# Kernel tuning notes

Measured on AMD Instinct MI355X. Metric: run time of the kernel, lower is better.

Reference implementation:

```python
import jax, jax.numpy as jnp
import numpy as np

MARGIN = 0.2
EPS = 1e-6  # F.pairwise_distance default eps (added to the difference)


def _cdist(x):
    # Euclidean pairwise distances, [N, N]
    sq = jnp.sum(x * x, axis=1)
    d2 = sq[:, None] + sq[None, :] - 2.0 * (x @ x.T)
    return jnp.sqrt(jnp.maximum(d2, 0.0))


def setup_inputs() -> dict:
    key = jax.random.key(0)
    k1, k2 = jax.random.split(key)
    features = jax.random.normal(k1, (8192, 128), dtype=jnp.float32)
    labels = jax.random.randint(k2, (8192,), 0, 512)
    return {"features": features, "labels": labels}


def reference(features, labels):
    # Distances are used only for (non-differentiable) index selection.
    dists = jax.lax.stop_gradient(_cdist(features))
    pos_mask = labels[None, :] == labels[:, None]  # includes diagonal (self), as in the torch loop
    neg_mask = ~pos_mask

    # Batch-hard mining, vectorized over all anchor rows:
    # hardest positive = max dist among same-label; hardest negative = min dist among different-label.
    pos_idx = jnp.argmax(jnp.where(pos_mask, dists, -jnp.inf), axis=1)
    neg_idx = jnp.argmin(jnp.where(neg_mask, dists, jnp.inf), axis=1)
    # Anchor is skipped in the original loop only if it has no negatives.
    valid = jnp.any(neg_mask, axis=1)

    anchors = features
    pos = features[pos_idx]
    neg = features[neg_idx]

    # F.pairwise_distance(x1, x2, p=2) == ||x1 - x2 + eps||_2
    pos_d = jnp.linalg.norm(anchors - pos + EPS, axis=1)
    neg_d = jnp.linalg.norm(anchors - neg + EPS, axis=1)
    per_anchor = jax.nn.relu(pos_d - neg_d + MARGIN)

    cnt = jnp.sum(valid)
    loss = jnp.where(
        cnt > 0,
        jnp.sum(jnp.where(valid, per_anchor, 0.0)) / jnp.maximum(cnt, 1).astype(per_anchor.dtype),
        jnp.zeros((), per_anchor.dtype),
    )
    return loss
```

## Files before the change

### kernel.cpp

```cpp
#include <hip/hip_runtime.h>
#include <hip/hip_bf16.h>

#define N 8192
#define DIMS 128
#define NSLICE 32
#define SLICE_COLS (N / NSLICE)
#define SUBTILES (SLICE_COLS / 16)
#define NSTEPS (SUBTILES / 2)
#define ROWS_PER_BLOCK 128
#define STRIPS 2
#define NROWBLK (N / ROWS_PER_BLOCK)
#define NFIN 2048
#define MARGIN_F 0.2f
#define EPS_F 1e-6f
#define META_LDS 16384
#define INF_F __builtin_huge_valf()

typedef __bf16 bf16x8 __attribute__((ext_vector_type(8)));
typedef float f32x4 __attribute__((ext_vector_type(4)));

#define XB_OFF   0
#define XNEG_OFF 2097152
#define META_OFF 4194304
#define PART_OFF 4259840
#define BSUM_OFF 6356992

#define GLD_LDS(g, l) \
  __builtin_amdgcn_global_load_lds( \
      (const __attribute__((address_space(1))) void*)(g), \
      (__attribute__((address_space(3))) void*)(l), 16, 0, 0)

__global__ __launch_bounds__(256) void prep_kernel(
    const float* __restrict__ feat, const int* __restrict__ lab,
    unsigned short* __restrict__ Xb, unsigned short* __restrict__ Xneg,
    float2* __restrict__ meta) {
  int row = blockIdx.x * 4 + (threadIdx.x >> 6);
  int lane = threadIdx.x & 63;
  float2 x = *reinterpret_cast<const float2*>(feat + (size_t)row * DIMS + lane * 2);
  __hip_bfloat16 hx = __float2bfloat16(x.x);
  __hip_bfloat16 hy = __float2bfloat16(x.y);
  unsigned short ux, uy;
  __builtin_memcpy(&ux, &hx, 2);
  __builtin_memcpy(&uy, &hy, 2);
  unsigned int packed = (unsigned int)ux | ((unsigned int)uy << 16);
  *reinterpret_cast<unsigned int*>(Xb + (size_t)row * DIMS + lane * 2) = packed;
  *reinterpret_cast<unsigned int*>(Xneg + (size_t)row * DIMS + lane * 2) =
      packed ^ 0x80008000u;
  float s = x.x * x.x + x.y * x.y;
#pragma unroll
  for (int m = 32; m >= 1; m >>= 1) s += __shfl_xor(s, m, 64);
  if (lane == 0)
    meta[row] = make_float2(0.5f * (s + 512.0f), __int_as_float(lab[row]));
}

__global__ __launch_bounds__(256, 4) void mine_kernel(
    const unsigned short* __restrict__ Xb, const unsigned short* __restrict__ Xneg,
    const float2* __restrict__ meta, const int* __restrict__ lab,
    uint2* __restrict__ part) {
  __shared__ char smem[2 * 8192 + 2048];

  int rb = blockIdx.x / NSLICE;
  int sl = blockIdx.x % NSLICE;
  int tid = threadIdx.x;
  int wave = tid >> 6;
  int lane = tid & 63;
  int lrow = lane & 15;
  int lk = lane >> 4;
  int rowbase = rb * ROWS_PER_BLOCK + wave * (STRIPS * 16);
  int j0 = sl * SLICE_COLS;

  if (wave < 2) {
    const char* g = (const char*)meta + (size_t)j0 * 8 + tid * 16;
    char* l = smem + META_LDS + wave * 1024;
    GLD_LDS(g, l);
  }
  int colt = tid >> 4;
  int chunk = tid & 15;
  const char* gsrc0 = (const char*)Xneg + (size_t)(j0 + colt) * 256 +
                      ((chunk ^ (colt & 7)) * 16);
  {
    GLD_LDS(gsrc0, smem + wave * 1024);
    GLD_LDS(gsrc0 + 4096, smem + 4096 + wave * 1024);
  }

  bf16x8 afrag[STRIPS][4];
#pragma unroll
  for (int s = 0; s < STRIPS; ++s) {
    const unsigned short* rp = Xb + (size_t)(rowbase + s * 16 + lrow) * DIMS;
#pragma unroll
    for (int g = 0; g < 4; ++g)
      afrag[s][g] = *reinterpret_cast<const bf16x8*>(rp + g * 32 + lk * 8);
  }
  int4 labi[STRIPS];
#pragma unroll
  for (int s = 0; s < STRIPS; ++s)
    labi[s] = *reinterpret_cast<const int4*>(lab + rowbase + s * 16 + lk * 4);

  unsigned int bpu[STRIPS][4], bnu[STRIPS][4];
#pragma unroll
  for (int s = 0; s < STRIPS; ++s)
#pragma unroll
    for (int e = 0; e < 4; ++e) { bpu[s][e] = 0u; bnu[s][e] = 0xFFFFFFFFu; }

  int boff[4];
#pragma unroll
  for (int g = 0; g < 4; ++g)
    boff[g] = lrow * 256 + (((g * 4 + lk) ^ (lrow & 7)) * 16);

  __syncthreads();

  for (int it = 0; it < NSTEPS; ++it) {
    int cur = it & 1;
    if (it + 1 < NSTEPS) {
      const char* g = gsrc0 + (size_t)(it + 1) * 8192;
      char* l = smem + (cur ^ 1) * 8192 + wave * 1024;
      GLD_LDS(g, l);
      GLD_LDS(g + 4096, l + 4096);
    }

#pragma unroll
    for (int h = 0; h < 2; ++h) {
      int t = it * 2 + h;
      float2 mcur =
          *reinterpret_cast<const float2*>(smem + META_LDS + t * 128 + lrow * 8);
      float hinit = mcur.x;
      int labj = __float_as_int(mcur.y);
      unsigned int ju = (unsigned int)(j0 + t * 16 + lrow);

      const char* bbase = smem + cur * 8192 + h * 4096;
      bf16x8 bb[4];
#pragma unroll
      for (int g = 0; g < 4; ++g)
        bb[g] = *reinterpret_cast<const bf16x8*>(bbase + boff[g]);

#pragma unroll
      for (int s = 0; s < STRIPS; ++s) {
        f32x4 acc = {hinit, hinit, hinit, hinit};
#pragma unroll
        for (int g = 0; g < 4; ++g)
          acc = __builtin_amdgcn_mfma_f32_16x16x32_bf16(afrag[s][g], bb[g], acc,
                                                        0, 0, 0);
        int labs[4] = {labi[s].x, labi[s].y, labi[s].z, labi[s].w};
#pragma unroll
        for (int e = 0; e < 4; ++e) {
          unsigned int u = (__float_as_uint(acc[e]) & 0xFFFFE000u) | ju;
          bool pos = (labj == labs[e]);
          unsigned int up = pos ? u : 0u;
          unsigned int un = pos ? 0xFFFFFFFFu : u;
          bpu[s][e] = max(bpu[s][e], up);
          bnu[s][e] = min(bnu[s][e], un);
        }
      }
    }
    __syncthreads();
  }

#pragma unroll
  for (int s = 0; s < STRIPS; ++s) {
#pragma unroll
    for (int e = 0; e < 4; ++e) {
      unsigned int pu = bpu[s][e], nu = bnu[s][e];
#pragma unroll
      for (int m = 1; m < 16; m <<= 1) {
        pu = max(pu, (unsigned int)__shfl_xor((int)pu, m, 64));
        nu = min(nu, (unsigned int)__shfl_xor((int)nu, m, 64));
      }
      if (lrow == 0) {
        int row = rowbase + s * 16 + lk * 4 + e;
        part[(size_t)sl * N + row] = make_uint2(pu, nu);
      }
    }
  }
}

__global__ __launch_bounds__(256) void finalize_kernel(
    const float* __restrict__ feat, const uint2* __restrict__ part,
    float2* __restrict__ bsum) {
  int wave = threadIdx.x >> 6, lane = threadIdx.x & 63;
  int i = blockIdx.x * 4 + wave;

  unsigned int pu = 0u, nu = 0xFFFFFFFFu;
  if (lane < NSLICE) {
    uint2 p = part[(size_t)lane * N + i];
    pu = p.x; nu = p.y;
  }
#pragma unroll
  for (int m = 1; m < NSLICE; m <<= 1) {
    pu = max(pu, (unsigned int)__shfl_xor((int)pu, m, 64));
    nu = min(nu, (unsigned int)__shfl_xor((int)nu, m, 64));
  }
  pu = (unsigned int)__shfl((int)pu, 0, 64);
  nu = (unsigned int)__shfl((int)nu, 0, 64);
  bool valid = (nu != 0xFFFFFFFFu);
  int pi = (int)(pu & 8191u);
  int ni = (int)(nu & 8191u);

  float2 av = *reinterpret_cast<const float2*>(feat + (size_t)i * DIMS + lane * 2);
  float2 pw = *reinterpret_cast<const float2*>(feat + (size_t)pi * DIMS + lane * 2);
  float2 nw = *reinterpret_cast<const float2*>(feat + (size_t)ni * DIMS + lane * 2);
  float d0 = av.x - pw.x + EPS_F, d1 = av.y - pw.y + EPS_F;
  float sp = fmaf(d0, d0, d1 * d1);
  float e0 = av.x - nw.x + EPS_F, e1 = av.y - nw.y + EPS_F;
  float sn = fmaf(e0, e0, e1 * e1);
#pragma unroll
  for (int m = 32; m >= 1; m >>= 1) {
    sp += __shfl_xor(sp, m, 64);
    sn += __shfl_xor(sn, m, 64);
  }

  __shared__ float s_s[4], s_c[4];
  if (lane == 0) {
    float per = sqrtf(sp) - sqrtf(sn) + MARGIN_F;
    per = per > 0.f ? per : 0.f;
    per = valid ? per : 0.f;
    s_s[wave] = per;
    s_c[wave] = valid ? 1.f : 0.f;
  }
  __syncthreads();
  if (threadIdx.x == 0) {
    float ts = (s_s[0] + s_s[1]) + (s_s[2] + s_s[3]);
    float tc = (s_c[0] + s_c[1]) + (s_c[2] + s_c[3]);
    bsum[blockIdx.x] = make_float2(ts, tc);
  }
}

__global__ __launch_bounds__(256) void final_reduce_kernel(
    const float2* __restrict__ bsum, float* __restrict__ out) {
  int t = threadIdx.x;
  float s = 0.f, c = 0.f;
#pragma unroll
  for (int k = 0; k < NFIN / 256; ++k) {
    float2 v = bsum[t + k * 256];
    s += v.x; c += v.y;
  }
#pragma unroll
  for (int m = 32; m >= 1; m >>= 1) {
    s += __shfl_xor(s, m, 64);
    c += __shfl_xor(c, m, 64);
  }
  __shared__ float s_s[4], s_c[4];
  int wave = t >> 6, lane = t & 63;
  if (lane == 0) { s_s[wave] = s; s_c[wave] = c; }
  __syncthreads();
  if (t == 0) {
    float ts = (s_s[0] + s_s[1]) + (s_s[2] + s_s[3]);
    float tc = (s_c[0] + s_c[1]) + (s_c[2] + s_c[3]);
    out[0] = (tc > 0.f) ? (ts / tc) : 0.f;
  }
}

extern "C" void kernel_launch(void* const* d_in, const int* in_sizes, int n_in,
                              void* d_out, int out_size, void* d_ws, size_t ws_size,
                              hipStream_t stream) {
  const float* feat = (const float*)d_in[0];
  const int* lab = (const int*)d_in[1];
  char* ws = (char*)d_ws;
  unsigned short* Xb = (unsigned short*)(ws + XB_OFF);
  unsigned short* Xneg = (unsigned short*)(ws + XNEG_OFF);
  float2* meta = (float2*)(ws + META_OFF);
  uint2* part = (uint2*)(ws + PART_OFF);
  float2* bsum = (float2*)(ws + BSUM_OFF);
  float* out = (float*)d_out;

  prep_kernel<<<N / 4, 256, 0, stream>>>(feat, lab, Xb, Xneg, meta);
  mine_kernel<<<NROWBLK * NSLICE, 256, 0, stream>>>(Xb, Xneg, meta, lab, part);
  finalize_kernel<<<N / 4, 256, 0, stream>>>(feat, part, bsum);
  final_reduce_kernel<<<1, 256, 0, stream>>>(bsum, out);
}
```

Baseline: 46.48 us.

## Exploit distance symmetry by mining only upper-triangular tiles with transposed reductions

The mining kernel now launches one block per upper-triangular 128x128 tile pair instead of covering the full matrix. Each MFMA result serves both the row-wise hardest positive/negative and, through a row/column norm swap, the column-wise transposed candidates. Transposed results are reduced through LDS and written as extra partials. This roughly halves the MFMA work, but adds ALU work, shuffles and LDS traffic per tile, and finalize now reduces 64 partials per row.

```diff
diff --git a/kernel.cpp b/kernel.cpp
--- a/kernel.cpp
+++ b/kernel.cpp
@@ -3,17 +3,17 @@
 
 #define N 8192
 #define DIMS 128
-#define NSLICE 32
-#define SLICE_COLS (N / NSLICE)
-#define SUBTILES (SLICE_COLS / 16)
-#define NSTEPS (SUBTILES / 2)
-#define ROWS_PER_BLOCK 128
+#define NT 64
+#define TILE 128
+#define NBLK (NT * (NT + 1) / 2)
+#define SUBTILES 8
+#define NSTEPS 4
 #define STRIPS 2
-#define NROWBLK (N / ROWS_PER_BLOCK)
 #define NFIN 2048
 #define MARGIN_F 0.2f
 #define EPS_F 1e-6f
-#define META_LDS 16384
+#define COLMETA_LDS 16384
+#define BUFT_LDS 17408
 #define INF_F __builtin_huge_valf()
 
 typedef __bf16 bf16x8 __attribute__((ext_vector_type(8)));
@@ -23,7 +23,7 @@
 #define XNEG_OFF 2097152
 #define META_OFF 4194304
 #define PART_OFF 4259840
-#define BSUM_OFF 6356992
+#define BSUM_OFF 8454144
 
 #define GLD_LDS(g, l) \
   __builtin_amdgcn_global_load_lds( \
@@ -55,23 +55,29 @@
 
 __global__ __launch_bounds__(256, 4) void mine_kernel(
     const unsigned short* __restrict__ Xb, const unsigned short* __restrict__ Xneg,
-    const float2* __restrict__ meta, const int* __restrict__ lab,
-    uint2* __restrict__ part) {
-  __shared__ char smem[2 * 8192 + 2048];
-
-  int rb = blockIdx.x / NSLICE;
-  int sl = blockIdx.x % NSLICE;
+    const float2* __restrict__ meta, uint2* __restrict__ part) {
+  __shared__ char smem[2 * 8192 + 1024 + 4096];
+
+  int k = blockIdx.x;
+  int rb = (int)floorf((float)NT + 0.5f -
+                       sqrtf(((float)NT + 0.5f) * ((float)NT + 0.5f) - 2.0f * (float)k));
+  if (rb < 0) rb = 0;
+  while (rb > 0 && rb * NT - rb * (rb - 1) / 2 > k) --rb;
+  while ((rb + 1) * NT - (rb + 1) * rb / 2 <= k) ++rb;
+  int cb = rb + (k - (rb * NT - rb * (rb - 1) / 2));
+  bool doT = (rb != cb);
+
   int tid = threadIdx.x;
   int wave = tid >> 6;
   int lane = tid & 63;
   int lrow = lane & 15;
   int lk = lane >> 4;
-  int rowbase = rb * ROWS_PER_BLOCK + wave * (STRIPS * 16);
-  int j0 = sl * SLICE_COLS;
-
-  if (wave < 2) {
+  int rowbase = rb * TILE + wave * (STRIPS * 16);
+  int j0 = cb * TILE;
+
+  if (tid < 64) {
     const char* g = (const char*)meta + (size_t)j0 * 8 + tid * 16;
-    char* l = smem + META_LDS + wave * 1024;
+    char* l = smem + COLMETA_LDS;
     GLD_LDS(g, l);
   }
   int colt = tid >> 4;
@@ -91,10 +97,16 @@
     for (int g = 0; g < 4; ++g)
       afrag[s][g] = *reinterpret_cast<const bf16x8*>(rp + g * 32 + lk * 8);
   }
-  int4 labi[STRIPS];
+  float hrow_[STRIPS][4];
+  int labr[STRIPS][4];
 #pragma unroll
   for (int s = 0; s < STRIPS; ++s)
-    labi[s] = *reinterpret_cast<const int4*>(lab + rowbase + s * 16 + lk * 4);
+#pragma unroll
+    for (int e = 0; e < 4; ++e) {
+      float2 rm = meta[rowbase + s * 16 + lk * 4 + e];
+      hrow_[s][e] = rm.x;
+      labr[s][e] = __float_as_int(rm.y);
+    }
 
   unsigned int bpu[STRIPS][4], bnu[STRIPS][4];
 #pragma unroll
@@ -121,11 +133,12 @@
 #pragma unroll
     for (int h = 0; h < 2; ++h) {
       int t = it * 2 + h;
-      float2 mcur =
-          *reinterpret_cast<const float2*>(smem + META_LDS + t * 128 + lrow * 8);
-      float hinit = mcur.x;
-      int labj = __float_as_int(mcur.y);
-      unsigned int ju = (unsigned int)(j0 + t * 16 + lrow);
+      int cloc = t * 16 + lrow;
+      float2 cm =
+          *reinterpret_cast<const float2*>(smem + COLMETA_LDS + cloc * 8);
+      float hcol = cm.x;
+      int labc = __float_as_int(cm.y);
+      unsigned int juc = (unsigned int)(j0 + cloc);
 
       const char* bbase = smem + cur * 8192 + h * 4096;
       bf16x8 bb[4];
@@ -133,24 +146,38 @@
       for (int g = 0; g < 4; ++g)
         bb[g] = *reinterpret_cast<const bf16x8*>(bbase + boff[g]);
 
+      unsigned int tpu = 0u, tnu = 0xFFFFFFFFu;
 #pragma unroll
       for (int s = 0; s < STRIPS; ++s) {
-        f32x4 acc = {hinit, hinit, hinit, hinit};
+        f32x4 acc = {hcol, hcol, hcol, hcol};
 #pragma unroll
         for (int g = 0; g < 4; ++g)
           acc = __builtin_amdgcn_mfma_f32_16x16x32_bf16(afrag[s][g], bb[g], acc,
                                                         0, 0, 0);
-        int labs[4] = {labi[s].x, labi[s].y, labi[s].z, labi[s].w};
 #pragma unroll
         for (int e = 0; e < 4; ++e) {
-          unsigned int u = (__float_as_uint(acc[e]) & 0xFFFFE000u) | ju;
-          bool pos = (labj == labs[e]);
+          bool pos = (labc == labr[s][e]);
+          unsigned int u = (__float_as_uint(acc[e]) & 0xFFFFE000u) | juc;
           unsigned int up = pos ? u : 0u;
           unsigned int un = pos ? 0xFFFFFFFFu : u;
           bpu[s][e] = max(bpu[s][e], up);
           bnu[s][e] = min(bnu[s][e], un);
+          float kT = acc[e] + (hrow_[s][e] - hcol);
+          unsigned int jur = (unsigned int)(rowbase + s * 16 + lk * 4 + e);
+          unsigned int uT = (__float_as_uint(kT) & 0xFFFFE000u) | jur;
+          unsigned int utp = pos ? uT : 0u;
+          unsigned int utn = pos ? 0xFFFFFFFFu : uT;
+          tpu = max(tpu, utp);
+          tnu = min(tnu, utn);
         }
       }
+      tpu = max(tpu, (unsigned int)__shfl_xor((int)tpu, 16, 64));
+      tnu = min(tnu, (unsigned int)__shfl_xor((int)tnu, 16, 64));
+      tpu = max(tpu, (unsigned int)__shfl_xor((int)tpu, 32, 64));
+      tnu = min(tnu, (unsigned int)__shfl_xor((int)tnu, 32, 64));
+      if (doT && lane < 16)
+        *reinterpret_cast<uint2*>(smem + BUFT_LDS + (wave * 128 + cloc) * 8) =
+            make_uint2(tpu, tnu);
     }
     __syncthreads();
   }
@@ -167,9 +194,19 @@
       }
       if (lrow == 0) {
         int row = rowbase + s * 16 + lk * 4 + e;
-        part[(size_t)sl * N + row] = make_uint2(pu, nu);
+        part[(size_t)cb * N + row] = make_uint2(pu, nu);
       }
     }
+  }
+
+  if (doT && tid < 128) {
+    uint2 a0 = *reinterpret_cast<uint2*>(smem + BUFT_LDS + (0 * 128 + tid) * 8);
+    uint2 a1 = *reinterpret_cast<uint2*>(smem + BUFT_LDS + (1 * 128 + tid) * 8);
+    uint2 a2 = *reinterpret_cast<uint2*>(smem + BUFT_LDS + (2 * 128 + tid) * 8);
+    uint2 a3 = *reinterpret_cast<uint2*>(smem + BUFT_LDS + (3 * 128 + tid) * 8);
+    unsigned int pu = max(max(a0.x, a1.x), max(a2.x, a3.x));
+    unsigned int nu = min(min(a0.y, a1.y), min(a2.y, a3.y));
+    part[(size_t)rb * N + j0 + tid] = make_uint2(pu, nu);
   }
 }
 
@@ -179,13 +216,10 @@
   int wave = threadIdx.x >> 6, lane = threadIdx.x & 63;
   int i = blockIdx.x * 4 + wave;
 
-  unsigned int pu = 0u, nu = 0xFFFFFFFFu;
-  if (lane < NSLICE) {
-    uint2 p = part[(size_t)lane * N + i];
-    pu = p.x; nu = p.y;
-  }
-#pragma unroll
-  for (int m = 1; m < NSLICE; m <<= 1) {
+  uint2 p = part[(size_t)lane * N + i];
+  unsigned int pu = p.x, nu = p.y;
+#pragma unroll
+  for (int m = 1; m < 64; m <<= 1) {
     pu = max(pu, (unsigned int)__shfl_xor((int)pu, m, 64));
     nu = min(nu, (unsigned int)__shfl_xor((int)nu, m, 64));
   }
@@ -263,7 +297,7 @@
   float* out = (float*)d_out;
 
   prep_kernel<<<N / 4, 256, 0, stream>>>(feat, lab, Xb, Xneg, meta);
-  mine_kernel<<<NROWBLK * NSLICE, 256, 0, stream>>>(Xb, Xneg, meta, lab, part);
+  mine_kernel<<<NBLK, 256, 0, stream>>>(Xb, Xneg, meta, part);
   finalize_kernel<<<N / 4, 256, 0, stream>>>(feat, part, bsum);
   final_reduce_kernel<<<1, 256, 0, stream>>>(bsum, out);
 }
```

After: 74.37 us. 60.0% more time.
